# Kernel tuning notes

Hardware: AMD Instinct MI355X
Metric: run time of the kernel (lower is better)

## Reference

```python
import jax, jax.numpy as jnp
import numpy as np

B, C, H, W = 8, 256, 64, 64
NH, KD, AG, PS, MIP = 8, 32, 64, 8, 8   # heads, key_dim, agent_num, pool_size, mip
EPS = 1e-5
SCALE = KD ** -0.5


def _bn(x, p):
    # p: [4, C] rows = (gamma, beta, mean, var); inference-mode BatchNorm2d, x: [B,C,H,W]
    g, b, m, v = p[0], p[1], p[2], p[3]
    inv = g * jax.lax.rsqrt(v + EPS)
    return x * inv[:, None, None] + (b - m * inv)[:, None, None]


def _conv1x1_bn(x, w, p):
    # 1x1 conv (no bias) + BN; act is Identity (the torch Conv act assignment is
    # overwritten by the else-branch, so even act='silu' ends up Identity)
    return _bn(jnp.einsum('bchw,oc->bohw', x, w), p)


def setup_inputs() -> dict:
    key = jax.random.key(0)
    ks = jax.random.split(key, 12)
    s = 0.05
    return {
        'x':       jax.random.normal(ks[0], (B, C, H, W), jnp.float32),
        'w_qkv':   jax.random.normal(ks[1], (3 * C, C), jnp.float32) * s,
        'bn_qkv':  jax.random.uniform(ks[2], (4, 3 * C), jnp.float32, 0.5, 1.5),
        'w_cv1':   jax.random.normal(ks[3], (MIP, C), jnp.float32) * s,
        'bn_cv1':  jax.random.uniform(ks[4], (4, MIP), jnp.float32, 0.5, 1.5),
        'w_cv2':   jax.random.normal(ks[5], (C, MIP), jnp.float32) * s,
        'bn_cv2':  jax.random.uniform(ks[6], (4, C), jnp.float32, 0.5, 1.5),
        'w_proj':  jax.random.normal(ks[7], (C, C), jnp.float32) * s,
        'bn_proj': jax.random.uniform(ks[8], (4, C), jnp.float32, 0.5, 1.5),
        'w_pe':    jax.random.normal(ks[9], (C, 1, 3, 3), jnp.float32) * s,
        'bn_pe':   jax.random.uniform(ks[10], (4, C), jnp.float32, 0.5, 1.5),
    }


def reference(x, w_qkv, bn_qkv, w_cv1, bn_cv1, w_cv2, bn_cv2,
              w_proj, bn_proj, w_pe, bn_pe):
    N = H * W
    qkv = _conv1x1_bn(x, w_qkv, bn_qkv)                     # [B,3C,H,W]
    q, k, v = jnp.split(qkv, 3, axis=1)                     # each [B,C,H,W]

    # direct == 'h': pool over W -> [B,C,H,1], SE-style gate via cv1->cv2, multiply
    a_k = k.mean(axis=3, keepdims=True)
    a_v = v.mean(axis=3, keepdims=True)
    k = _conv1x1_bn(_conv1x1_bn(a_k, w_cv1, bn_cv1), w_cv2, bn_cv2) * k
    v = _conv1x1_bn(_conv1x1_bn(a_v, w_cv1, bn_cv1), w_cv2, bn_cv2) * v

    # agent tokens: AdaptiveAvgPool2d to (PS,PS) == block-mean since H,W % PS == 0
    ap = q.reshape(B, C, PS, H // PS, PS, W // PS).mean(axis=(3, 5))  # [B,C,PS,PS]
    a = ap.reshape(B, NH, KD, AG)                            # [B,h,d,agent]

    qr = q.reshape(B, NH, KD, N)
    kr = k.reshape(B, NH, KD, N)
    vr = v.reshape(B, NH, KD, N)

    attn_k = jax.nn.softmax(jnp.einsum('bhda,bhdn->bhan', a, kr) * SCALE, axis=-1)  # [B,h,agent,N]
    attn = jnp.einsum('bhan,bhdn->bhad', attn_k, vr)                                # [B,h,agent,d]
    q_attn = jax.nn.softmax(jnp.einsum('bhdn,bhda->bhna', qr, a) * SCALE, axis=-1)  # [B,h,N,agent]
    out = jnp.einsum('bhna,bhad->bhdn', q_attn, attn).reshape(B, C, H, W)

    # depthwise 3x3 positional encoding on v, then BN
    pe = jax.lax.conv_general_dilated(
        v, w_pe, window_strides=(1, 1), padding='SAME',
        dimension_numbers=('NCHW', 'OIHW', 'NCHW'), feature_group_count=C)
    out = out + _bn(pe, bn_pe)

    return _conv1x1_bn(out, w_proj, bn_proj)
```

## Files before the change

kernel.cpp:

```cpp
#include <hip/hip_runtime.h>
#include <hip/hip_bf16.h>

#define NB 8
#define NC 256
#define NHW 4096
#define HDIM 64
#define WDIM 64
#define NHEAD 8
#define NKD 32
#define NAG 64
#define NMIP 8
#define NSPLIT 16
#define EPSF 1e-5f
#define FSCALE 0.17677669529663687f
#define SZQ ((size_t)NB * NC * NHW)

typedef __attribute__((ext_vector_type(8))) short bf16x8;
typedef __attribute__((ext_vector_type(8))) unsigned short u16x8;
typedef __attribute__((ext_vector_type(4))) float f32x4;

__device__ __forceinline__ unsigned short f2bf(float f) {
    union { float f; unsigned u; } v; v.f = f;
    unsigned r = v.u + 0x7FFF + ((v.u >> 16) & 1);
    return (unsigned short)(r >> 16);
}
__device__ __forceinline__ float b2f(unsigned short u) {
    union { unsigned u32; float f; } v; v.u32 = ((unsigned)u) << 16; return v.f;
}

__global__ __launch_bounds__(256) void k_qkv(const float* __restrict__ x,
                                             const float* __restrict__ w,
                                             const float* __restrict__ bnp,
                                             unsigned short* __restrict__ Qb,
                                             unsigned short* __restrict__ Kb,
                                             unsigned short* __restrict__ Vb) {
    const int b   = blockIdx.z;
    const int ocB = blockIdx.y * 128;
    const int nB  = blockIdx.x * 128;
    const int tid = threadIdx.x;
    const int wv  = tid >> 6, lane = tid & 63;
    const int wm = wv >> 1, wn = wv & 1;
    const int lm = lane & 15, lg = lane >> 4;

    __shared__ unsigned short As[128 * 40];
    __shared__ unsigned short Bs[128 * 40];
    __shared__ float inv_s[128], bias_s[128];

    if (tid < 128) {
        int oc = ocB + tid;
        float g = bnp[0 * 768 + oc], be = bnp[1 * 768 + oc];
        float m = bnp[2 * 768 + oc], vv = bnp[3 * 768 + oc];
        float inv = g * rsqrtf(vv + EPSF);
        inv_s[tid] = inv;
        bias_s[tid] = be - m * inv;
    }

    f32x4 acc[4][4];
    #pragma unroll
    for (int i = 0; i < 4; ++i)
        #pragma unroll
        for (int j = 0; j < 4; ++j)
            acc[i][j] = (f32x4){0.f, 0.f, 0.f, 0.f};

    const int arow = tid >> 1, akh = (tid & 1) * 16;
    const int bn_ = tid & 127, bkh = (tid >> 7) * 16;

    for (int k0 = 0; k0 < 256; k0 += 32) {
        {
            const float* wp = w + (size_t)(ocB + arow) * 256 + k0 + akh;
            float4 f0 = reinterpret_cast<const float4*>(wp)[0];
            float4 f1 = reinterpret_cast<const float4*>(wp)[1];
            float4 f2 = reinterpret_cast<const float4*>(wp)[2];
            float4 f3 = reinterpret_cast<const float4*>(wp)[3];
            union { unsigned short u[16]; bf16x8 v[2]; } pk;
            pk.u[0]=f2bf(f0.x); pk.u[1]=f2bf(f0.y); pk.u[2]=f2bf(f0.z); pk.u[3]=f2bf(f0.w);
            pk.u[4]=f2bf(f1.x); pk.u[5]=f2bf(f1.y); pk.u[6]=f2bf(f1.z); pk.u[7]=f2bf(f1.w);
            pk.u[8]=f2bf(f2.x); pk.u[9]=f2bf(f2.y); pk.u[10]=f2bf(f2.z); pk.u[11]=f2bf(f2.w);
            pk.u[12]=f2bf(f3.x); pk.u[13]=f2bf(f3.y); pk.u[14]=f2bf(f3.z); pk.u[15]=f2bf(f3.w);
            *reinterpret_cast<bf16x8*>(&As[arow * 40 + akh]) = pk.v[0];
            *reinterpret_cast<bf16x8*>(&As[arow * 40 + akh + 8]) = pk.v[1];
        }
        {
            const float* xp = x + ((size_t)b * NC + k0 + bkh) * NHW + nB + bn_;
            float t[16];
            #pragma unroll
            for (int i = 0; i < 16; ++i) t[i] = xp[(size_t)i * NHW];
            union { unsigned short u[16]; bf16x8 v[2]; } pk;
            #pragma unroll
            for (int i = 0; i < 16; ++i) pk.u[i] = f2bf(t[i]);
            *reinterpret_cast<bf16x8*>(&Bs[bn_ * 40 + bkh]) = pk.v[0];
            *reinterpret_cast<bf16x8*>(&Bs[bn_ * 40 + bkh + 8]) = pk.v[1];
        }
        __syncthreads();

        bf16x8 af[4], bfr[4];
        #pragma unroll
        for (int mi = 0; mi < 4; ++mi)
            af[mi] = *reinterpret_cast<const bf16x8*>(&As[(wm * 64 + mi * 16 + lm) * 40 + lg * 8]);
        #pragma unroll
        for (int ni = 0; ni < 4; ++ni)
            bfr[ni] = *reinterpret_cast<const bf16x8*>(&Bs[(wn * 64 + ni * 16 + lm) * 40 + lg * 8]);
        #pragma unroll
        for (int mi = 0; mi < 4; ++mi)
            #pragma unroll
            for (int ni = 0; ni < 4; ++ni)
                acc[mi][ni] = __builtin_amdgcn_mfma_f32_16x16x32_bf16(af[mi], bfr[ni], acc[mi][ni], 0, 0, 0);
        __syncthreads();
    }

    #pragma unroll
    for (int mi = 0; mi < 4; ++mi) {
        #pragma unroll
        for (int r = 0; r < 4; ++r) {
            int lo = wm * 64 + mi * 16 + lg * 4 + r;
            int oc = ocB + lo;
            float inv = inv_s[lo], bias = bias_s[lo];
            unsigned short* base; int oc2;
            if (oc < 256)      { base = Qb; oc2 = oc; }
            else if (oc < 512) { base = Kb; oc2 = oc - 256; }
            else               { base = Vb; oc2 = oc - 512; }
            unsigned short* dp = base + ((size_t)b * NC + oc2) * NHW + nB;
            #pragma unroll
            for (int ni = 0; ni < 4; ++ni) {
                int n = wn * 64 + ni * 16 + lm;
                dp[n] = f2bf(acc[mi][ni][r] * inv + bias);
            }
        }
    }
}

__global__ __launch_bounds__(256) void k_means(const unsigned short* __restrict__ K,
                                               const unsigned short* __restrict__ V,
                                               float* __restrict__ AMK,
                                               float* __restrict__ AMV) {
    const int bc = blockIdx.x;
    const int b = bc >> 8;
    const int c = bc & 255;
    const int t = threadIdx.x;
    #pragma unroll
    for (int pass = 0; pass < 2; ++pass) {
        const unsigned short* p = (pass ? V : K) + (size_t)bc * NHW + t * 16;
        u16x8 a0 = *reinterpret_cast<const u16x8*>(p);
        u16x8 a1 = *reinterpret_cast<const u16x8*>(p + 8);
        float s = 0.f;
        #pragma unroll
        for (int i = 0; i < 8; ++i) s += b2f(a0[i]);
        #pragma unroll
        for (int i = 0; i < 8; ++i) s += b2f(a1[i]);
        s += __shfl_xor(s, 1);
        s += __shfl_xor(s, 2);
        if ((t & 3) == 0)
            (pass ? AMV : AMK)[((size_t)b * HDIM + (t >> 2)) * NC + c] = s * (1.0f / 64.0f);
    }
}

__global__ __launch_bounds__(256) void k_gatecomp(const float* __restrict__ AMK,
                                                  const float* __restrict__ AMV,
                                                  const float* __restrict__ w1,
                                                  const float* __restrict__ bn1,
                                                  const float* __restrict__ w2,
                                                  const float* __restrict__ bn2,
                                                  float* __restrict__ GK,
                                                  float* __restrict__ GV) {
    const int b = blockIdx.x >> 6;
    const int h = blockIdx.x & 63;
    const int c = threadIdx.x;
    __shared__ float am[NC];
    __shared__ float m1[NMIP];
    for (int pass = 0; pass < 2; ++pass) {
        am[c] = (pass ? AMV : AMK)[((size_t)b * HDIM + h) * NC + c];
        __syncthreads();
        if (c < NMIP) {
            float t = 0.f;
            for (int cc = 0; cc < NC; ++cc) t += w1[c * NC + cc] * am[cc];
            float g = bn1[0 * NMIP + c], be = bn1[1 * NMIP + c];
            float mm = bn1[2 * NMIP + c], vv = bn1[3 * NMIP + c];
            float inv = g * rsqrtf(vv + EPSF);
            m1[c] = t * inv + (be - mm * inv);
        }
        __syncthreads();
        {
            float t = 0.f;
            #pragma unroll
            for (int j = 0; j < NMIP; ++j) t += w2[c * NMIP + j] * m1[j];
            float g = bn2[0 * NC + c], be = bn2[1 * NC + c];
            float mm = bn2[2 * NC + c], vv = bn2[3 * NC + c];
            float inv = g * rsqrtf(vv + EPSF);
            (pass ? GV : GK)[((size_t)b * NC + c) * HDIM + h] = t * inv + (be - mm * inv);
        }
        __syncthreads();
    }
}

__global__ __launch_bounds__(64) void k_pool(const unsigned short* __restrict__ Q,
                                             float* __restrict__ A_) {
    const int bc = blockIdx.x;
    const int ag = threadIdx.x;
    const int ph = ag >> 3, pw = ag & 7;
    const unsigned short* src = Q + (size_t)bc * NHW;
    float s = 0.f;
    #pragma unroll
    for (int i = 0; i < 8; ++i) {
        u16x8 v = *reinterpret_cast<const u16x8*>(&src[(ph * 8 + i) * WDIM + pw * 8]);
        #pragma unroll
        for (int j = 0; j < 8; ++j) s += b2f(v[j]);
    }
    A_[(size_t)bc * NAG + ag] = s * (1.0f / 64.0f);
}

__global__ __launch_bounds__(256) void k_attn_part(const unsigned short* __restrict__ K,
                                                   const unsigned short* __restrict__ V,
                                                   const float* __restrict__ A_,
                                                   const float* __restrict__ GK,
                                                   const float* __restrict__ GV,
                                                   float* __restrict__ Pm,
                                                   float* __restrict__ Pl,
                                                   float* __restrict__ Pacc) {
    const int bh = blockIdx.x >> 4;
    const int ns = blockIdx.x & (NSPLIT - 1);
    const int b = bh >> 3, h = bh & 7;
    const int tid = threadIdx.x;
    const int wv = tid >> 6, lane = tid & 63;
    const int lm = lane & 15, lg = lane >> 4;

    __shared__ unsigned short a_s[64 * 40];
    __shared__ unsigned short kt_s[64 * 40];
    __shared__ unsigned short vt_s[32 * 72];
    __shared__ unsigned short Ps[64 * 72];

    {
        int d = tid >> 3, ag0 = (tid & 7) * 8;
        const float* ap = A_ + ((size_t)(b * NC + h * NKD + d)) * NAG + ag0;
        float4 v0 = reinterpret_cast<const float4*>(ap)[0];
        float4 v1 = reinterpret_cast<const float4*>(ap)[1];
        float t8[8] = {v0.x, v0.y, v0.z, v0.w, v1.x, v1.y, v1.z, v1.w};
        #pragma unroll
        for (int i = 0; i < 8; ++i)
            a_s[(ag0 + i) * 40 + d] = f2bf(t8[i] * FSCALE);
    }

    float mrow[4], lrow[4];
    f32x4 acc[2];
    #pragma unroll
    for (int r = 0; r < 4; ++r) { mrow[r] = -1e30f; lrow[r] = 0.f; }
    acc[0] = (f32x4){0.f, 0.f, 0.f, 0.f};
    acc[1] = (f32x4){0.f, 0.f, 0.f, 0.f};

    const int colbase = ns * (NHW / NSPLIT);
    const unsigned short* Kp = K + (size_t)(b * NC + h * NKD) * NHW + colbase;
    const unsigned short* Vp = V + (size_t)(b * NC + h * NKD) * NHW + colbase;
    const int sd = tid >> 3;
    const size_t gbase = ((size_t)(b * NC + h * NKD + sd)) * HDIM;
    __syncthreads();

    for (int nt = 0; nt < 4; ++nt) {
        const int gh = ns * 4 + nt;
        {
            int c0 = tid & 7;
            float gk = GK[gbase + gh];
            const unsigned short* kp = Kp + (size_t)sd * NHW + nt * 64 + c0;
            #pragma unroll
            for (int i = 0; i < 8; ++i)
                kt_s[(c0 + 8 * i) * 40 + sd] = f2bf(b2f(kp[8 * i]) * gk);
        }
        {
            int c0 = (tid & 7) * 8;
            float gv = GV[gbase + gh];
            const unsigned short* vp = Vp + (size_t)sd * NHW + nt * 64 + c0;
            u16x8 vr = *reinterpret_cast<const u16x8*>(vp);
            union { unsigned short u[8]; bf16x8 v; } pk;
            #pragma unroll
            for (int i = 0; i < 8; ++i) pk.u[i] = f2bf(b2f(vr[i]) * gv);
            *reinterpret_cast<bf16x8*>(&vt_s[sd * 72 + c0]) = pk.v;
        }
        __syncthreads();

        f32x4 s[4];
        {
            bf16x8 af = *reinterpret_cast<const bf16x8*>(&a_s[(wv * 16 + lm) * 40 + lg * 8]);
            #pragma unroll
            for (int ni = 0; ni < 4; ++ni) {
                bf16x8 kf = *reinterpret_cast<const bf16x8*>(&kt_s[(ni * 16 + lm) * 40 + lg * 8]);
                s[ni] = __builtin_amdgcn_mfma_f32_16x16x32_bf16(
                    af, kf, (f32x4){0.f, 0.f, 0.f, 0.f}, 0, 0, 0);
            }
        }

        float fsc[4];
        #pragma unroll
        for (int r = 0; r < 4; ++r) {
            float mx = fmaxf(fmaxf(s[0][r], s[1][r]), fmaxf(s[2][r], s[3][r]));
            mx = fmaxf(mx, __shfl_xor(mx, 1));
            mx = fmaxf(mx, __shfl_xor(mx, 2));
            mx = fmaxf(mx, __shfl_xor(mx, 4));
            mx = fmaxf(mx, __shfl_xor(mx, 8));
            float mnew = fmaxf(mrow[r], mx);
            fsc[r] = __expf(mrow[r] - mnew);
            mrow[r] = mnew;
            int agrow = wv * 16 + lg * 4 + r;
            float ps = 0.f;
            #pragma unroll
            for (int ni = 0; ni < 4; ++ni) {
                float p = __expf(s[ni][r] - mnew);
                Ps[agrow * 72 + ni * 16 + lm] = f2bf(p);
                ps += p;
            }
            ps += __shfl_xor(ps, 1);
            ps += __shfl_xor(ps, 2);
            ps += __shfl_xor(ps, 4);
            ps += __shfl_xor(ps, 8);
            lrow[r] = lrow[r] * fsc[r] + ps;
        }
        #pragma unroll
        for (int ni = 0; ni < 2; ++ni)
            #pragma unroll
            for (int r = 0; r < 4; ++r)
                acc[ni][r] *= fsc[r];
        __syncthreads();

        #pragma unroll
        for (int kk = 0; kk < 2; ++kk) {
            bf16x8 pa = *reinterpret_cast<const bf16x8*>(&Ps[(wv * 16 + lm) * 72 + kk * 32 + lg * 8]);
            #pragma unroll
            for (int ni = 0; ni < 2; ++ni) {
                bf16x8 vb = *reinterpret_cast<const bf16x8*>(&vt_s[(ni * 16 + lm) * 72 + kk * 32 + lg * 8]);
                acc[ni] = __builtin_amdgcn_mfma_f32_16x16x32_bf16(pa, vb, acc[ni], 0, 0, 0);
            }
        }
        __syncthreads();
    }

    const size_t pbase = (size_t)(bh * NSPLIT + ns) * NAG;
    #pragma unroll
    for (int r = 0; r < 4; ++r) {
        int ag = wv * 16 + lg * 4 + r;
        #pragma unroll
        for (int ni = 0; ni < 2; ++ni)
            Pacc[(pbase + ag) * NKD + ni * 16 + lm] = acc[ni][r];
        if (lm == 0) {
            Pm[pbase + ag] = mrow[r];
            Pl[pbase + ag] = lrow[r];
        }
    }
}

__global__ __launch_bounds__(256) void k_attn_comb(const float* __restrict__ Pm,
                                                   const float* __restrict__ Pl,
                                                   const float* __restrict__ Pacc,
                                                   float* __restrict__ AT) {
    const int bh = blockIdx.x;
    const int tid = threadIdx.x;
    const int ag = tid >> 2, jg = tid & 3;
    float m = -1e30f;
    #pragma unroll
    for (int ns = 0; ns < NSPLIT; ++ns)
        m = fmaxf(m, Pm[(size_t)(bh * NSPLIT + ns) * NAG + ag]);
    float l = 0.f;
    float acc[8] = {};
    for (int ns = 0; ns < NSPLIT; ++ns) {
        size_t pb = (size_t)(bh * NSPLIT + ns) * NAG + ag;
        float f = __expf(Pm[pb] - m);
        l += Pl[pb] * f;
        const float* pp = Pacc + pb * NKD + jg * 8;
        #pragma unroll
        for (int i = 0; i < 8; ++i) acc[i] += pp[i] * f;
    }
    float linv = 1.0f / l;
    #pragma unroll
    for (int i = 0; i < 8; ++i)
        AT[((size_t)bh * NAG + ag) * NKD + jg * 8 + i] = acc[i] * linv;
}

__global__ __launch_bounds__(256) void k_qattn(const unsigned short* __restrict__ Q,
                                               const float* __restrict__ A_,
                                               const float* __restrict__ AT,
                                               float* __restrict__ O1) {
    const int bh = blockIdx.y;
    const int b = bh >> 3, h = bh & 7;
    const int n0 = blockIdx.x * 128;
    const int tid = threadIdx.x;
    const int wv = tid >> 6, lane = tid & 63;
    const int lm = lane & 15, lg = lane >> 4;

    __shared__ unsigned short Qs[128][40];
    __shared__ unsigned short Ags[64][40];
    __shared__ unsigned short ATs[32][72];
    __shared__ unsigned short Ps[128][72];

    const unsigned short* Qbase = Q + ((size_t)b * NC + h * NKD) * NHW;

    {
        int d = tid >> 3, nb_ = (tid & 7) * 16;
        const unsigned short* qp = Qbase + (size_t)d * NHW + n0 + nb_;
        u16x8 v0 = *reinterpret_cast<const u16x8*>(qp);
        u16x8 v1 = *reinterpret_cast<const u16x8*>(qp + 8);
        #pragma unroll
        for (int i = 0; i < 8; ++i) Qs[nb_ + i][d] = v0[i];
        #pragma unroll
        for (int i = 0; i < 8; ++i) Qs[nb_ + 8 + i][d] = v1[i];
    }
    if (tid < 128) {
        int d = tid >> 2, ag0 = (tid & 3) * 16;
        const float* ap = A_ + ((size_t)(b * NC + h * NKD + d)) * NAG + ag0;
        #pragma unroll
        for (int i = 0; i < 16; ++i) Ags[ag0 + i][d] = f2bf(ap[i] * FSCALE);
    }
    if (tid < 128) {
        int ag = tid >> 1, d0 = (tid & 1) * 16;
        const float* atp = AT + ((size_t)bh * NAG + ag) * NKD + d0;
        #pragma unroll
        for (int i = 0; i < 16; ++i) ATs[d0 + i][ag] = f2bf(atp[i]);
    }
    __syncthreads();

    f32x4 s[2][4];
    #pragma unroll
    for (int mi = 0; mi < 2; ++mi)
        #pragma unroll
        for (int ni = 0; ni < 4; ++ni)
            s[mi][ni] = (f32x4){0.f, 0.f, 0.f, 0.f};
    {
        bf16x8 qa[2], ab[4];
        #pragma unroll
        for (int mi = 0; mi < 2; ++mi)
            qa[mi] = *reinterpret_cast<const bf16x8*>(&Qs[wv * 32 + mi * 16 + lm][lg * 8]);
        #pragma unroll
        for (int ni = 0; ni < 4; ++ni)
            ab[ni] = *reinterpret_cast<const bf16x8*>(&Ags[ni * 16 + lm][lg * 8]);
        #pragma unroll
        for (int mi = 0; mi < 2; ++mi)
            #pragma unroll
            for (int ni = 0; ni < 4; ++ni)
                s[mi][ni] = __builtin_amdgcn_mfma_f32_16x16x32_bf16(qa[mi], ab[ni], s[mi][ni], 0, 0, 0);
    }

    float lsum[2][4];
    #pragma unroll
    for (int mi = 0; mi < 2; ++mi) {
        #pragma unroll
        for (int r = 0; r < 4; ++r) {
            float mx = fmaxf(fmaxf(s[mi][0][r], s[mi][1][r]), fmaxf(s[mi][2][r], s[mi][3][r]));
            mx = fmaxf(mx, __shfl_xor(mx, 1));
            mx = fmaxf(mx, __shfl_xor(mx, 2));
            mx = fmaxf(mx, __shfl_xor(mx, 4));
            mx = fmaxf(mx, __shfl_xor(mx, 8));
            int nrow = wv * 32 + mi * 16 + lg * 4 + r;
            float ls = 0.f;
            #pragma unroll
            for (int ni = 0; ni < 4; ++ni) {
                float p = __expf(s[mi][ni][r] - mx);
                ls += p;
                Ps[nrow][ni * 16 + lm] = f2bf(p);
            }
            ls += __shfl_xor(ls, 1);
            ls += __shfl_xor(ls, 2);
            ls += __shfl_xor(ls, 4);
            ls += __shfl_xor(ls, 8);
            lsum[mi][r] = ls;
        }
    }
    __syncthreads();

    f32x4 o[2][2];
    #pragma unroll
    for (int mi = 0; mi < 2; ++mi)
        #pragma unroll
        for (int ni = 0; ni < 2; ++ni)
            o[mi][ni] = (f32x4){0.f, 0.f, 0.f, 0.f};
    #pragma unroll
    for (int kk = 0; kk < 2; ++kk) {
        bf16x8 pa[2], vb[2];
        #pragma unroll
        for (int mi = 0; mi < 2; ++mi)
            pa[mi] = *reinterpret_cast<const bf16x8*>(&Ps[wv * 32 + mi * 16 + lm][kk * 32 + lg * 8]);
        #pragma unroll
        for (int ni = 0; ni < 2; ++ni)
            vb[ni] = *reinterpret_cast<const bf16x8*>(&ATs[ni * 16 + lm][kk * 32 + lg * 8]);
        #pragma unroll
        for (int mi = 0; mi < 2; ++mi)
            #pragma unroll
            for (int ni = 0; ni < 2; ++ni)
                o[mi][ni] = __builtin_amdgcn_mfma_f32_16x16x32_bf16(pa[mi], vb[ni], o[mi][ni], 0, 0, 0);
    }

    float* obase = O1 + ((size_t)b * NC + h * NKD) * NHW + n0;
    #pragma unroll
    for (int mi = 0; mi < 2; ++mi) {
        #pragma unroll
        for (int r = 0; r < 4; ++r) {
            float rl = 1.0f / lsum[mi][r];
            int n = wv * 32 + mi * 16 + lg * 4 + r;
            #pragma unroll
            for (int ni = 0; ni < 2; ++ni) {
                int d = ni * 16 + lm;
                obase[(size_t)d * NHW + n] = o[mi][ni][r] * rl;
            }
        }
    }
}

__global__ __launch_bounds__(256) void k_pe(const unsigned short* __restrict__ V,
                                            const float* __restrict__ GV,
                                            const float* __restrict__ wpe,
                                            const float* __restrict__ bnp,
                                            float* __restrict__ O1) {
    const int bc = blockIdx.x;
    const int c = bc & (NC - 1);
    __shared__ float gv_s[HDIM];
    if (threadIdx.x < HDIM) gv_s[threadIdx.x] = GV[(size_t)bc * HDIM + threadIdx.x];
    float wreg[9];
    #pragma unroll
    for (int i = 0; i < 9; ++i) wreg[i] = wpe[c * 9 + i];
    float g = bnp[0 * NC + c], be = bnp[1 * NC + c];
    float m = bnp[2 * NC + c], vv = bnp[3 * NC + c];
    float inv = g * rsqrtf(vv + EPSF);
    float bias = be - m * inv;
    const unsigned short* src = V + (size_t)bc * NHW;
    float* dst = O1 + (size_t)bc * NHW;
    __syncthreads();
    for (int idx = threadIdx.x; idx < NHW; idx += 256) {
        int h = idx >> 6, w = idx & 63;
        float s = 0.f;
        #pragma unroll
        for (int kh = 0; kh < 3; ++kh) {
            int hh = h + kh - 1;
            if (hh < 0 || hh >= HDIM) continue;
            float rs = 0.f;
            #pragma unroll
            for (int kw = 0; kw < 3; ++kw) {
                int ww = w + kw - 1;
                if (ww < 0 || ww >= WDIM) continue;
                rs = fmaf(wreg[kh * 3 + kw], b2f(src[hh * WDIM + ww]), rs);
            }
            s = fmaf(rs, gv_s[hh], s);
        }
        dst[idx] += s * inv + bias;
    }
}

__global__ __launch_bounds__(256) void k_proj(const float* __restrict__ O1,
                                              const float* __restrict__ w,
                                              const float* __restrict__ bnp,
                                              float* __restrict__ out) {
    const int b   = blockIdx.z;
    const int ocB = blockIdx.y * 128;
    const int nB  = blockIdx.x * 128;
    const int tid = threadIdx.x;
    const int wv  = tid >> 6, lane = tid & 63;
    const int wm = wv >> 1, wn = wv & 1;
    const int lm = lane & 15, lg = lane >> 4;

    __shared__ unsigned short As[128 * 40];
    __shared__ unsigned short Bs[128 * 40];
    __shared__ float inv_s[128], bias_s[128];

    if (tid < 128) {
        int oc = ocB + tid;
        float g = bnp[0 * NC + oc], be = bnp[1 * NC + oc];
        float m = bnp[2 * NC + oc], vv = bnp[3 * NC + oc];
        float inv = g * rsqrtf(vv + EPSF);
        inv_s[tid] = inv;
        bias_s[tid] = be - m * inv;
    }

    f32x4 acc[4][4];
    #pragma unroll
    for (int i = 0; i < 4; ++i)
        #pragma unroll
        for (int j = 0; j < 4; ++j)
            acc[i][j] = (f32x4){0.f, 0.f, 0.f, 0.f};

    const int arow = tid >> 1, akh = (tid & 1) * 16;
    const int bn_ = tid & 127, bkh = (tid >> 7) * 16;

    for (int k0 = 0; k0 < 256; k0 += 32) {
        {
            const float* wp = w + (size_t)(ocB + arow) * 256 + k0 + akh;
            float4 f0 = reinterpret_cast<const float4*>(wp)[0];
            float4 f1 = reinterpret_cast<const float4*>(wp)[1];
            float4 f2 = reinterpret_cast<const float4*>(wp)[2];
            float4 f3 = reinterpret_cast<const float4*>(wp)[3];
            union { unsigned short u[16]; bf16x8 v[2]; } pk;
            pk.u[0]=f2bf(f0.x); pk.u[1]=f2bf(f0.y); pk.u[2]=f2bf(f0.z); pk.u[3]=f2bf(f0.w);
            pk.u[4]=f2bf(f1.x); pk.u[5]=f2bf(f1.y); pk.u[6]=f2bf(f1.z); pk.u[7]=f2bf(f1.w);
            pk.u[8]=f2bf(f2.x); pk.u[9]=f2bf(f2.y); pk.u[10]=f2bf(f2.z); pk.u[11]=f2bf(f2.w);
            pk.u[12]=f2bf(f3.x); pk.u[13]=f2bf(f3.y); pk.u[14]=f2bf(f3.z); pk.u[15]=f2bf(f3.w);
            *reinterpret_cast<bf16x8*>(&As[arow * 40 + akh]) = pk.v[0];
            *reinterpret_cast<bf16x8*>(&As[arow * 40 + akh + 8]) = pk.v[1];
        }
        {
            const float* xp = O1 + ((size_t)b * NC + k0 + bkh) * NHW + nB + bn_;
            float t[16];
            #pragma unroll
            for (int i = 0; i < 16; ++i) t[i] = xp[(size_t)i * NHW];
            union { unsigned short u[16]; bf16x8 v[2]; } pk;
            #pragma unroll
            for (int i = 0; i < 16; ++i) pk.u[i] = f2bf(t[i]);
            *reinterpret_cast<bf16x8*>(&Bs[bn_ * 40 + bkh]) = pk.v[0];
            *reinterpret_cast<bf16x8*>(&Bs[bn_ * 40 + bkh + 8]) = pk.v[1];
        }
        __syncthreads();

        bf16x8 af[4], bfr[4];
        #pragma unroll
        for (int mi = 0; mi < 4; ++mi)
            af[mi] = *reinterpret_cast<const bf16x8*>(&As[(wm * 64 + mi * 16 + lm) * 40 + lg * 8]);
        #pragma unroll
        for (int ni = 0; ni < 4; ++ni)
            bfr[ni] = *reinterpret_cast<const bf16x8*>(&Bs[(wn * 64 + ni * 16 + lm) * 40 + lg * 8]);
        #pragma unroll
        for (int mi = 0; mi < 4; ++mi)
            #pragma unroll
            for (int ni = 0; ni < 4; ++ni)
                acc[mi][ni] = __builtin_amdgcn_mfma_f32_16x16x32_bf16(af[mi], bfr[ni], acc[mi][ni], 0, 0, 0);
        __syncthreads();
    }

    float* dstb = out + ((size_t)b * NC + ocB) * NHW + nB;
    #pragma unroll
    for (int mi = 0; mi < 4; ++mi) {
        int lo_base = wm * 64 + mi * 16 + lg * 4;
        #pragma unroll
        for (int r = 0; r < 4; ++r) {
            int lo = lo_base + r;
            float inv = inv_s[lo], bias = bias_s[lo];
            #pragma unroll
            for (int ni = 0; ni < 4; ++ni) {
                int n = wn * 64 + ni * 16 + lm;
                dstb[(size_t)lo * NHW + n] = acc[mi][ni][r] * inv + bias;
            }
        }
    }
}

extern "C" void kernel_launch(void* const* d_in, const int* in_sizes, int n_in,
                              void* d_out, int out_size, void* d_ws, size_t ws_size,
                              hipStream_t stream) {
    (void)in_sizes; (void)n_in; (void)out_size; (void)ws_size;
    const float* x       = (const float*)d_in[0];
    const float* w_qkv   = (const float*)d_in[1];
    const float* bn_qkv  = (const float*)d_in[2];
    const float* w_cv1   = (const float*)d_in[3];
    const float* bn_cv1  = (const float*)d_in[4];
    const float* w_cv2   = (const float*)d_in[5];
    const float* bn_cv2  = (const float*)d_in[6];
    const float* w_proj  = (const float*)d_in[7];
    const float* bn_proj = (const float*)d_in[8];
    const float* w_pe    = (const float*)d_in[9];
    const float* bn_pe   = (const float*)d_in[10];
    float* out = (float*)d_out;

    unsigned short* Qb = (unsigned short*)d_ws;
    unsigned short* Kb = Qb + SZQ;
    unsigned short* Vb = Kb + SZQ;
    float* O1   = (float*)(Vb + SZQ);
    float* Aa   = O1 + SZQ;
    float* AT   = Aa + (size_t)NB * NC * NAG;
    float* Pm   = AT + (size_t)NB * NHEAD * NAG * NKD;
    float* Pl   = Pm + (size_t)NB * NHEAD * NSPLIT * NAG;
    float* Pacc = Pl + (size_t)NB * NHEAD * NSPLIT * NAG;
    float* AMK  = Pacc + (size_t)NB * NHEAD * NSPLIT * NAG * NKD;
    float* AMV  = AMK + (size_t)NB * HDIM * NC;
    float* GK   = AMV + (size_t)NB * HDIM * NC;
    float* GV   = GK + (size_t)NB * NC * HDIM;

    k_qkv<<<dim3(32, 6, NB), 256, 0, stream>>>(x, w_qkv, bn_qkv, Qb, Kb, Vb);
    k_means<<<NB * NC, 256, 0, stream>>>(Kb, Vb, AMK, AMV);
    k_gatecomp<<<NB * HDIM, 256, 0, stream>>>(AMK, AMV, w_cv1, bn_cv1, w_cv2, bn_cv2, GK, GV);
    k_pool<<<NB * NC, 64, 0, stream>>>(Qb, Aa);
    k_attn_part<<<NB * NHEAD * NSPLIT, 256, 0, stream>>>(Kb, Vb, Aa, GK, GV, Pm, Pl, Pacc);
    k_attn_comb<<<NB * NHEAD, 256, 0, stream>>>(Pm, Pl, Pacc, AT);
    k_qattn<<<dim3(32, 64), 256, 0, stream>>>(Qb, Aa, AT, O1);
    k_pe<<<NB * NC, 256, 0, stream>>>(Vb, GV, w_pe, bn_pe, O1);
    k_proj<<<dim3(32, 2, NB), 256, 0, stream>>>(O1, w_proj, bn_proj, out);
}
```

Before: 169.4 us.

## Pre-cast weights to bf16, stage x once per QKV block, store O1 as bf16

Adds a small kernel that converts the QKV and projection weights to bf16 once per call, so the GEMM kernels no longer convert fp32 weights on every tile. The QKV kernel now stages the whole 256-channel x tile in shared memory once and loops over three 128-row output chunks, so x is read from global memory fewer times. The attention output buffer O1 becomes bf16, halving its write and read traffic in qattn, pe and proj. The costs are an extra launch, a larger LDS footprint in k_qkv (about 78KB) that can lower occupancy, and extra bf16 rounding of the intermediate output.

```diff
diff --git a/kernel.cpp b/kernel.cpp
--- a/kernel.cpp
+++ b/kernel.cpp
@@ -17,6 +17,7 @@
 
 typedef __attribute__((ext_vector_type(8))) short bf16x8;
 typedef __attribute__((ext_vector_type(8))) unsigned short u16x8;
+typedef __attribute__((ext_vector_type(4))) unsigned short u16x4;
 typedef __attribute__((ext_vector_type(4))) float f32x4;
 
 __device__ __forceinline__ unsigned short f2bf(float f) {
@@ -28,102 +29,120 @@
     union { unsigned u32; float f; } v; v.u32 = ((unsigned)u) << 16; return v.f;
 }
 
+__global__ __launch_bounds__(256) void k_wcast(const float* __restrict__ wq,
+                                               const float* __restrict__ wp,
+                                               unsigned short* __restrict__ wqb,
+                                               unsigned short* __restrict__ wpb) {
+    const int i = (blockIdx.x * 256 + threadIdx.x) * 4;
+    const int NQ = 768 * 256;
+    if (i < NQ) {
+        float4 v = *reinterpret_cast<const float4*>(wq + i);
+        u16x4 u = {f2bf(v.x), f2bf(v.y), f2bf(v.z), f2bf(v.w)};
+        *reinterpret_cast<u16x4*>(wqb + i) = u;
+    } else {
+        int j = i - NQ;
+        float4 v = *reinterpret_cast<const float4*>(wp + j);
+        u16x4 u = {f2bf(v.x), f2bf(v.y), f2bf(v.z), f2bf(v.w)};
+        *reinterpret_cast<u16x4*>(wpb + j) = u;
+    }
+}
+
 __global__ __launch_bounds__(256) void k_qkv(const float* __restrict__ x,
-                                             const float* __restrict__ w,
+                                             const unsigned short* __restrict__ wb,
                                              const float* __restrict__ bnp,
                                              unsigned short* __restrict__ Qb,
                                              unsigned short* __restrict__ Kb,
                                              unsigned short* __restrict__ Vb) {
-    const int b   = blockIdx.z;
-    const int ocB = blockIdx.y * 128;
-    const int nB  = blockIdx.x * 128;
+    const int b  = blockIdx.z;
+    const int nB = blockIdx.x * 128;
+    const int p0 = blockIdx.y * 3;
     const int tid = threadIdx.x;
-    const int wv  = tid >> 6, lane = tid & 63;
+    const int wv = tid >> 6, lane = tid & 63;
     const int wm = wv >> 1, wn = wv & 1;
     const int lm = lane & 15, lg = lane >> 4;
 
+    __shared__ unsigned short Bs[128 * 264];
     __shared__ unsigned short As[128 * 40];
-    __shared__ unsigned short Bs[128 * 40];
-    __shared__ float inv_s[128], bias_s[128];
-
-    if (tid < 128) {
-        int oc = ocB + tid;
-        float g = bnp[0 * 768 + oc], be = bnp[1 * 768 + oc];
-        float m = bnp[2 * 768 + oc], vv = bnp[3 * 768 + oc];
-        float inv = g * rsqrtf(vv + EPSF);
-        inv_s[tid] = inv;
-        bias_s[tid] = be - m * inv;
-    }
-
-    f32x4 acc[4][4];
-    #pragma unroll
-    for (int i = 0; i < 4; ++i)
-        #pragma unroll
-        for (int j = 0; j < 4; ++j)
-            acc[i][j] = (f32x4){0.f, 0.f, 0.f, 0.f};
+
+    {
+        const int nq = (tid & 31) * 4;
+        const int ks = (tid >> 5) * 32;
+        const float* xp = x + ((size_t)b * NC + ks) * NHW + nB + nq;
+        #pragma unroll
+        for (int ch = 0; ch < 4; ++ch) {
+            float4 v[8];
+            #pragma unroll
+            for (int i = 0; i < 8; ++i)
+                v[i] = *reinterpret_cast<const float4*>(xp + (size_t)(ch * 8 + i) * NHW);
+            #pragma unroll
+            for (int j = 0; j < 4; ++j) {
+                union { unsigned short u[8]; u16x8 w8; } pk;
+                #pragma unroll
+                for (int i = 0; i < 8; ++i) {
+                    float f = (j == 0) ? v[i].x : (j == 1) ? v[i].y : (j == 2) ? v[i].z : v[i].w;
+                    pk.u[i] = f2bf(f);
+                }
+                *reinterpret_cast<u16x8*>(&Bs[(nq + j) * 264 + ks + ch * 8]) = pk.w8;
+            }
+        }
+    }
 
     const int arow = tid >> 1, akh = (tid & 1) * 16;
-    const int bn_ = tid & 127, bkh = (tid >> 7) * 16;
-
-    for (int k0 = 0; k0 < 256; k0 += 32) {
-        {
-            const float* wp = w + (size_t)(ocB + arow) * 256 + k0 + akh;
-            float4 f0 = reinterpret_cast<const float4*>(wp)[0];
-            float4 f1 = reinterpret_cast<const float4*>(wp)[1];
-            float4 f2 = reinterpret_cast<const float4*>(wp)[2];
-            float4 f3 = reinterpret_cast<const float4*>(wp)[3];
-            union { unsigned short u[16]; bf16x8 v[2]; } pk;
-            pk.u[0]=f2bf(f0.x); pk.u[1]=f2bf(f0.y); pk.u[2]=f2bf(f0.z); pk.u[3]=f2bf(f0.w);
-            pk.u[4]=f2bf(f1.x); pk.u[5]=f2bf(f1.y); pk.u[6]=f2bf(f1.z); pk.u[7]=f2bf(f1.w);
-            pk.u[8]=f2bf(f2.x); pk.u[9]=f2bf(f2.y); pk.u[10]=f2bf(f2.z); pk.u[11]=f2bf(f2.w);
-            pk.u[12]=f2bf(f3.x); pk.u[13]=f2bf(f3.y); pk.u[14]=f2bf(f3.z); pk.u[15]=f2bf(f3.w);
-            *reinterpret_cast<bf16x8*>(&As[arow * 40 + akh]) = pk.v[0];
-            *reinterpret_cast<bf16x8*>(&As[arow * 40 + akh + 8]) = pk.v[1];
-        }
-        {
-            const float* xp = x + ((size_t)b * NC + k0 + bkh) * NHW + nB + bn_;
-            float t[16];
-            #pragma unroll
-            for (int i = 0; i < 16; ++i) t[i] = xp[(size_t)i * NHW];
-            union { unsigned short u[16]; bf16x8 v[2]; } pk;
-            #pragma unroll
-            for (int i = 0; i < 16; ++i) pk.u[i] = f2bf(t[i]);
-            *reinterpret_cast<bf16x8*>(&Bs[bn_ * 40 + bkh]) = pk.v[0];
-            *reinterpret_cast<bf16x8*>(&Bs[bn_ * 40 + bkh + 8]) = pk.v[1];
-        }
-        __syncthreads();
-
-        bf16x8 af[4], bfr[4];
-        #pragma unroll
-        for (int mi = 0; mi < 4; ++mi)
-            af[mi] = *reinterpret_cast<const bf16x8*>(&As[(wm * 64 + mi * 16 + lm) * 40 + lg * 8]);
-        #pragma unroll
-        for (int ni = 0; ni < 4; ++ni)
-            bfr[ni] = *reinterpret_cast<const bf16x8*>(&Bs[(wn * 64 + ni * 16 + lm) * 40 + lg * 8]);
-        #pragma unroll
-        for (int mi = 0; mi < 4; ++mi)
+
+    for (int pp = 0; pp < 3; ++pp) {
+        const int ocB = (p0 + pp) * 128;
+        f32x4 acc[4][4];
+        #pragma unroll
+        for (int i = 0; i < 4; ++i)
+            #pragma unroll
+            for (int j = 0; j < 4; ++j)
+                acc[i][j] = (f32x4){0.f, 0.f, 0.f, 0.f};
+
+        for (int k0 = 0; k0 < 256; k0 += 32) {
+            __syncthreads();
+            {
+                const unsigned short* wp = wb + (size_t)(ocB + arow) * 256 + k0 + akh;
+                u16x8 a0 = *reinterpret_cast<const u16x8*>(wp);
+                u16x8 a1 = *reinterpret_cast<const u16x8*>(wp + 8);
+                *reinterpret_cast<u16x8*>(&As[arow * 40 + akh]) = a0;
+                *reinterpret_cast<u16x8*>(&As[arow * 40 + akh + 8]) = a1;
+            }
+            __syncthreads();
+
+            bf16x8 af[4], bfr[4];
+            #pragma unroll
+            for (int mi = 0; mi < 4; ++mi)
+                af[mi] = *reinterpret_cast<const bf16x8*>(&As[(wm * 64 + mi * 16 + lm) * 40 + lg * 8]);
             #pragma unroll
             for (int ni = 0; ni < 4; ++ni)
-                acc[mi][ni] = __builtin_amdgcn_mfma_f32_16x16x32_bf16(af[mi], bfr[ni], acc[mi][ni], 0, 0, 0);
-        __syncthreads();
-    }
-
-    #pragma unroll
-    for (int mi = 0; mi < 4; ++mi) {
-        #pragma unroll
-        for (int r = 0; r < 4; ++r) {
-            int lo = wm * 64 + mi * 16 + lg * 4 + r;
-            int oc = ocB + lo;
-            float inv = inv_s[lo], bias = bias_s[lo];
-            unsigned short* base; int oc2;
-            if (oc < 256)      { base = Qb; oc2 = oc; }
-            else if (oc < 512) { base = Kb; oc2 = oc - 256; }
-            else               { base = Vb; oc2 = oc - 512; }
-            unsigned short* dp = base + ((size_t)b * NC + oc2) * NHW + nB;
-            #pragma unroll
-            for (int ni = 0; ni < 4; ++ni) {
-                int n = wn * 64 + ni * 16 + lm;
-                dp[n] = f2bf(acc[mi][ni][r] * inv + bias);
+                bfr[ni] = *reinterpret_cast<const bf16x8*>(&Bs[(wn * 64 + ni * 16 + lm) * 264 + k0 + lg * 8]);
+            #pragma unroll
+            for (int mi = 0; mi < 4; ++mi)
+                #pragma unroll
+                for (int ni = 0; ni < 4; ++ni)
+                    acc[mi][ni] = __builtin_amdgcn_mfma_f32_16x16x32_bf16(af[mi], bfr[ni], acc[mi][ni], 0, 0, 0);
+        }
+
+        #pragma unroll
+        for (int mi = 0; mi < 4; ++mi) {
+            #pragma unroll
+            for (int r = 0; r < 4; ++r) {
+                int lo = wm * 64 + mi * 16 + lg * 4 + r;
+                int oc = ocB + lo;
+                float g = bnp[0 * 768 + oc], be = bnp[1 * 768 + oc];
+                float m = bnp[2 * 768 + oc], vv = bnp[3 * 768 + oc];
+                float inv = g * rsqrtf(vv + EPSF);
+                float bias = be - m * inv;
+                unsigned short* base; int oc2;
+                if (oc < 256)      { base = Qb; oc2 = oc; }
+                else if (oc < 512) { base = Kb; oc2 = oc - 256; }
+                else               { base = Vb; oc2 = oc - 512; }
+                unsigned short* dp = base + ((size_t)b * NC + oc2) * NHW + nB;
+                #pragma unroll
+                for (int ni = 0; ni < 4; ++ni) {
+                    int n = wn * 64 + ni * 16 + lm;
+                    dp[n] = f2bf(acc[mi][ni][r] * inv + bias);
+                }
             }
         }
     }
@@ -268,10 +287,10 @@
             float gv = GV[gbase + gh];
             const unsigned short* vp = Vp + (size_t)sd * NHW + nt * 64 + c0;
             u16x8 vr = *reinterpret_cast<const u16x8*>(vp);
-            union { unsigned short u[8]; bf16x8 v; } pk;
+            union { unsigned short u[8]; u16x8 v; } pk;
             #pragma unroll
             for (int i = 0; i < 8; ++i) pk.u[i] = f2bf(b2f(vr[i]) * gv);
-            *reinterpret_cast<bf16x8*>(&vt_s[sd * 72 + c0]) = pk.v;
+            *reinterpret_cast<u16x8*>(&vt_s[sd * 72 + c0]) = pk.v;
         }
         __syncthreads();
 
@@ -374,7 +393,7 @@
 __global__ __launch_bounds__(256) void k_qattn(const unsigned short* __restrict__ Q,
                                                const float* __restrict__ A_,
                                                const float* __restrict__ AT,
-                                               float* __restrict__ O1) {
+                                               unsigned short* __restrict__ O1) {
     const int bh = blockIdx.y;
     const int b = bh >> 3, h = bh & 7;
     const int n0 = blockIdx.x * 128;
@@ -483,7 +502,7 @@
                 o[mi][ni] = __builtin_amdgcn_mfma_f32_16x16x32_bf16(pa[mi], vb[ni], o[mi][ni], 0, 0, 0);
     }
 
-    float* obase = O1 + ((size_t)b * NC + h * NKD) * NHW + n0;
+    unsigned short* obase = O1 + ((size_t)b * NC + h * NKD) * NHW + n0;
     #pragma unroll
     for (int mi = 0; mi < 2; ++mi) {
         #pragma unroll
@@ -493,7 +512,7 @@
             #pragma unroll
             for (int ni = 0; ni < 2; ++ni) {
                 int d = ni * 16 + lm;
-                obase[(size_t)d * NHW + n] = o[mi][ni][r] * rl;
+                obase[(size_t)d * NHW + n] = f2bf(o[mi][ni][r] * rl);
             }
         }
     }
@@ -503,7 +522,7 @@
                                             const float* __restrict__ GV,
                                             const float* __restrict__ wpe,
                                             const float* __restrict__ bnp,
-                                            float* __restrict__ O1) {
+                                            unsigned short* __restrict__ O1) {
     const int bc = blockIdx.x;
     const int c = bc & (NC - 1);
     __shared__ float gv_s[HDIM];
@@ -516,7 +535,7 @@
     float inv = g * rsqrtf(vv + EPSF);
     float bias = be - m * inv;
     const unsigned short* src = V + (size_t)bc * NHW;
-    float* dst = O1 + (size_t)bc * NHW;
+    unsigned short* dst = O1 + (size_t)bc * NHW;
     __syncthreads();
     for (int idx = threadIdx.x; idx < NHW; idx += 256) {
         int h = idx >> 6, w = idx & 63;
@@ -534,12 +553,12 @@
             }
             s = fmaf(rs, gv_s[hh], s);
         }
-        dst[idx] += s * inv + bias;
-    }
-}
-
-__global__ __launch_bounds__(256) void k_proj(const float* __restrict__ O1,
-                                              const float* __restrict__ w,
+        dst[idx] = f2bf(b2f(dst[idx]) + s * inv + bias);
+    }
+}
+
+__global__ __launch_bounds__(256) void k_proj(const unsigned short* __restrict__ O1,
+                                              const unsigned short* __restrict__ wb,
                                               const float* __restrict__ bnp,
                                               float* __restrict__ out) {
     const int b   = blockIdx.z;
@@ -575,29 +594,19 @@
 
     for (int k0 = 0; k0 < 256; k0 += 32) {
         {
-            const float* wp = w + (size_t)(ocB + arow) * 256 + k0 + akh;
-            float4 f0 = reinterpret_cast<const float4*>(wp)[0];
-            float4 f1 = reinterpret_cast<const float4*>(wp)[1];
-            float4 f2 = reinterpret_cast<const float4*>(wp)[2];
-            float4 f3 = reinterpret_cast<const float4*>(wp)[3];
-            union { unsigned short u[16]; bf16x8 v[2]; } pk;
-            pk.u[0]=f2bf(f0.x); pk.u[1]=f2bf(f0.y); pk.u[2]=f2bf(f0.z); pk.u[3]=f2bf(f0.w);
-            pk.u[4]=f2bf(f1.x); pk.u[5]=f2bf(f1.y); pk.u[6]=f2bf(f1.z); pk.u[7]=f2bf(f1.w);
-            pk.u[8]=f2bf(f2.x); pk.u[9]=f2bf(f2.y); pk.u[10]=f2bf(f2.z); pk.u[11]=f2bf(f2.w);
-            pk.u[12]=f2bf(f3.x); pk.u[13]=f2bf(f3.y); pk.u[14]=f2bf(f3.z); pk.u[15]=f2bf(f3.w);
-            *reinterpret_cast<bf16x8*>(&As[arow * 40 + akh]) = pk.v[0];
-            *reinterpret_cast<bf16x8*>(&As[arow * 40 + akh + 8]) = pk.v[1];
+            const unsigned short* wp = wb + (size_t)(ocB + arow) * 256 + k0 + akh;
+            u16x8 a0 = *reinterpret_cast<const u16x8*>(wp);
+            u16x8 a1 = *reinterpret_cast<const u16x8*>(wp + 8);
+            *reinterpret_cast<u16x8*>(&As[arow * 40 + akh]) = a0;
+            *reinterpret_cast<u16x8*>(&As[arow * 40 + akh + 8]) = a1;
         }
         {
-            const float* xp = O1 + ((size_t)b * NC + k0 + bkh) * NHW + nB + bn_;
-            float t[16];
-            #pragma unroll
-            for (int i = 0; i < 16; ++i) t[i] = xp[(size_t)i * NHW];
-            union { unsigned short u[16]; bf16x8 v[2]; } pk;
-            #pragma unroll
-            for (int i = 0; i < 16; ++i) pk.u[i] = f2bf(t[i]);
-            *reinterpret_cast<bf16x8*>(&Bs[bn_ * 40 + bkh]) = pk.v[0];
-            *reinterpret_cast<bf16x8*>(&Bs[bn_ * 40 + bkh + 8]) = pk.v[1];
+            const unsigned short* xp = O1 + ((size_t)b * NC + k0 + bkh) * NHW + nB + bn_;
+            union { unsigned short u[16]; u16x8 v[2]; } pk;
+            #pragma unroll
+            for (int i = 0; i < 16; ++i) pk.u[i] = xp[(size_t)i * NHW];
+            *reinterpret_cast<u16x8*>(&Bs[bn_ * 40 + bkh]) = pk.v[0];
+            *reinterpret_cast<u16x8*>(&Bs[bn_ * 40 + bkh + 8]) = pk.v[1];
         }
         __syncthreads();
 
@@ -650,11 +659,13 @@
     const float* bn_pe   = (const float*)d_in[10];
     float* out = (float*)d_out;
 
-    unsigned short* Qb = (unsigned short*)d_ws;
-    unsigned short* Kb = Qb + SZQ;
-    unsigned short* Vb = Kb + SZQ;
-    float* O1   = (float*)(Vb + SZQ);
-    float* Aa   = O1 + SZQ;
+    unsigned short* Qb  = (unsigned short*)d_ws;
+    unsigned short* Kb  = Qb + SZQ;
+    unsigned short* Vb  = Kb + SZQ;
+    unsigned short* O1b = Vb + SZQ;
+    unsigned short* wqb = O1b + SZQ;
+    unsigned short* wpb = wqb + 768 * 256;
+    float* Aa   = (float*)(wpb + 65536);
     float* AT   = Aa + (size_t)NB * NC * NAG;
     float* Pm   = AT + (size_t)NB * NHEAD * NAG * NKD;
     float* Pl   = Pm + (size_t)NB * NHEAD * NSPLIT * NAG;
@@ -664,13 +675,14 @@
     float* GK   = AMV + (size_t)NB * HDIM * NC;
     float* GV   = GK + (size_t)NB * NC * HDIM;
 
-    k_qkv<<<dim3(32, 6, NB), 256, 0, stream>>>(x, w_qkv, bn_qkv, Qb, Kb, Vb);
+    k_wcast<<<256, 256, 0, stream>>>(w_qkv, w_proj, wqb, wpb);
+    k_qkv<<<dim3(32, 2, NB), 256, 0, stream>>>(x, wqb, bn_qkv, Qb, Kb, Vb);
     k_means<<<NB * NC, 256, 0, stream>>>(Kb, Vb, AMK, AMV);
     k_gatecomp<<<NB * HDIM, 256, 0, stream>>>(AMK, AMV, w_cv1, bn_cv1, w_cv2, bn_cv2, GK, GV);
     k_pool<<<NB * NC, 64, 0, stream>>>(Qb, Aa);
     k_attn_part<<<NB * NHEAD * NSPLIT, 256, 0, stream>>>(Kb, Vb, Aa, GK, GV, Pm, Pl, Pacc);
     k_attn_comb<<<NB * NHEAD, 256, 0, stream>>>(Pm, Pl, Pacc, AT);
-    k_qattn<<<dim3(32, 64), 256, 0, stream>>>(Qb, Aa, AT, O1);
-    k_pe<<<NB * NC, 256, 0, stream>>>(Vb, GV, w_pe, bn_pe, O1);
-    k_proj<<<dim3(32, 2, NB), 256, 0, stream>>>(O1, w_proj, bn_proj, out);
-}
+    k_qattn<<<dim3(32, 64), 256, 0, stream>>>(Qb, Aa, AT, O1b);
+    k_pe<<<NB * NC, 256, 0, stream>>>(Vb, GV, w_pe, bn_pe, O1b);
+    k_proj<<<dim3(32, 2, NB), 256, 0, stream>>>(O1b, wpb, bn_proj, out);
+}
```

After: 175.7 us. 1.04x slower.
